# Kernel optimization log

Measured on AMD Instinct MI355X. Metric: run time of the kernel, lower is better.

Reference implementation:

```python
import jax, jax.numpy as jnp
import numpy as np

B, D, T = 32, 1024, 1000
LMAX = 200
VOCAB = 80
BLANK = VOCAB - 1
NEG = -1e30


def setup_inputs() -> dict:
    key = jax.random.key(0)
    ks = jax.random.split(key, 8)
    decoder_outputs = jax.random.normal(ks[0], (B, D, T), dtype=jnp.float32)
    target_text = jax.random.randint(ks[1], (B, LMAX), 0, BLANK, dtype=jnp.int32)
    decoder_lengths = jax.random.randint(ks[2], (B,), T // 2, T + 1, dtype=jnp.int32)
    target_lengths = jax.random.randint(ks[3], (B,), 1, LMAX + 1, dtype=jnp.int32)
    # learned params (dropout is identity in eval / deterministic reference)
    W1 = jax.random.normal(ks[4], (D, D), dtype=jnp.float32) * (1.0 / np.sqrt(D))
    b1 = jnp.zeros((D,), dtype=jnp.float32)
    W2 = jax.random.normal(ks[5], (D, VOCAB), dtype=jnp.float32) * (1.0 / np.sqrt(D))
    b2 = jnp.zeros((VOCAB,), dtype=jnp.float32)
    return {"decoder_outputs": decoder_outputs, "target_text": target_text,
            "decoder_lengths": decoder_lengths, "target_lengths": target_lengths,
            "W1": W1, "b1": b1, "W2": W2, "b2": b2}


def _ctc_nll(log_probs, targets, input_lengths, target_lengths):
    # log_probs: [T, B, V]; standard CTC alpha (forward) DP over extended labels.
    Tt, Bb, V = log_probs.shape
    L = targets.shape[1]
    S = 2 * L + 1
    ext = jnp.full((Bb, S), BLANK, dtype=targets.dtype).at[:, 1::2].set(targets)
    ext_m2 = jnp.pad(ext, ((0, 0), (2, 0)), constant_values=BLANK)[:, :S]
    allow_skip = (ext != BLANK) & (ext != ext_m2)
    allow_skip = allow_skip.at[:, :2].set(False)

    lp0 = log_probs[0]  # [B, V]
    alpha0 = jnp.full((Bb, S), NEG, dtype=log_probs.dtype)
    alpha0 = alpha0.at[:, 0].set(lp0[:, BLANK])
    alpha0 = alpha0.at[:, 1].set(jnp.take_along_axis(lp0, targets[:, :1], axis=1)[:, 0])

    def step(alpha, inp):
        lp_t, t = inp
        emit = jnp.take_along_axis(lp_t, ext, axis=1)  # [B, S]
        a2 = jnp.pad(alpha, ((0, 0), (1, 0)), constant_values=NEG)[:, :S]
        a3 = jnp.pad(alpha, ((0, 0), (2, 0)), constant_values=NEG)[:, :S]
        a3 = jnp.where(allow_skip, a3, NEG)
        new = jnp.logaddexp(jnp.logaddexp(alpha, a2), a3) + emit
        alpha = jnp.where((t < input_lengths)[:, None], new, alpha)
        return alpha, None

    alpha, _ = jax.lax.scan(step, alpha0, (log_probs[1:], jnp.arange(1, Tt)))
    i1 = (2 * target_lengths - 1)[:, None]
    i2 = (2 * target_lengths)[:, None]
    last = jnp.logaddexp(jnp.take_along_axis(alpha, i1, axis=1)[:, 0],
                         jnp.take_along_axis(alpha, i2, axis=1)[:, 0])
    nll = -last
    # zero_infinity=True: invalid alignments -> 0 loss
    return jnp.where(last > NEG / 2, nll, 0.0)


def reference(decoder_outputs, target_text, decoder_lengths, target_lengths, W1, b1, W2, b2):
    x = jnp.transpose(decoder_outputs, (0, 2, 1))          # [B, T, D]
    h = jax.nn.relu(jnp.einsum('btd,de->bte', x, W1) + b1)  # proj + ReLU (dropout=identity)
    logits = jnp.einsum('btd,dv->btv', h, W2) + b2          # [B, T, V]
    log_probs = jax.nn.log_softmax(logits, axis=2)
    log_probs = jnp.transpose(log_probs, (1, 0, 2))         # [T, B, V]
    ctc_loss = _ctc_nll(log_probs, target_text, decoder_lengths, target_lengths)
    return (ctc_loss / decoder_lengths.astype(jnp.float32)).mean()
```

## Files before the change

### kernel.cpp

```cpp
#include <hip/hip_runtime.h>
#include <cstdint>
#include <cstddef>

#define BN_ 32
#define DD_ 1024
#define TT_ 1000
#define LMAX_ 200
#define VC_ 80
#define BLANK_ 79
#define SS_ 401
#define SPAD 512
#define NEGV (-1e30f)

typedef _Float16 half8 __attribute__((ext_vector_type(8)));
typedef float f32x4 __attribute__((ext_vector_type(4)));

__device__ __forceinline__ void async16(const void* g, void* l) {
  __builtin_amdgcn_global_load_lds(
      (const __attribute__((address_space(1))) unsigned int*)g,
      (__attribute__((address_space(3))) unsigned int*)l, 16, 0, 0);
}

__global__ __launch_bounds__(256) void transpose_all_kernel(
    const float* __restrict__ dec, const float* __restrict__ W1,
    const float* __restrict__ W2, _Float16* __restrict__ Af,
    _Float16* __restrict__ W1T, _Float16* __restrict__ W2T) {
  __shared__ _Float16 T[64][72];
  int z = blockIdx.z;
  const float* in; _Float16* out; int C;
  const int R = 1024;
  if (z < 32) {
    in = dec + (size_t)z * R * TT_;
    out = Af + (size_t)z * TT_ * R;
    C = TT_;
  } else if (z == 32) {
    in = W1; out = W1T; C = 1024;
  } else {
    in = W2; out = W2T; C = VC_;
  }
  int c0 = blockIdx.x * 64, r0 = blockIdx.y * 64;
  if (c0 >= C) return;
  int tid = threadIdx.x;
  int cl = tid & 63, rg = tid >> 6;
  int c = c0 + cl;
  bool cv = (c < C);
  const float* ip = in + (size_t)(r0 + rg * 16) * C + c;
  _Float16 h[16];
#pragma unroll
  for (int i = 0; i < 16; ++i) h[i] = cv ? (_Float16)ip[(size_t)i * C] : (_Float16)0.f;
  *(half8*)&T[cl][rg * 16] = *(half8*)&h[0];
  *(half8*)&T[cl][rg * 16 + 8] = *(half8*)&h[8];
  __syncthreads();
  int cr = tid >> 2, rc = (tid & 3) * 16;
  if (c0 + cr < C) {
    half8 a = *(const half8*)&T[cr][rc];
    half8 b2 = *(const half8*)&T[cr][rc + 8];
    _Float16* op = out + (size_t)(c0 + cr) * R + r0 + rc;
    *(half8*)op = a;
    *(half8*)(op + 8) = b2;
  }
}

__device__ __forceinline__ void stage_half(const _Float16* __restrict__ X,
                                           int x0, int kt, int h,
                                           _Float16* lds, int tid, int K) {
#pragma unroll
  for (int jj = 0; jj < 2; ++jj) {
    int seg = tid + 512 * jj;
    int row = seg >> 3, slot = seg & 7;
    int cg = slot ^ (row & 7);
    async16(X + (size_t)(x0 + h * 128 + row) * K + kt * 64 + cg * 8,
            lds + seg * 8);
  }
}

__global__ __launch_bounds__(512, 2) void gemm_relu_kernel(
    const _Float16* __restrict__ A, const _Float16* __restrict__ Bt,
    const float* __restrict__ bias, _Float16* __restrict__ H,
    int M, int N, int K) {
  __shared__ __align__(16) _Float16 sA[2][16384];
  __shared__ __align__(16) _Float16 sB[2][16384];
  int tid = threadIdx.x;
  int wave = tid >> 6, lane = tid & 63;
  int quad = lane >> 4, r16 = lane & 15;
  int wm = wave >> 2, wn = wave & 3;

  int orig = blockIdx.x, nwg = gridDim.x;
  int xcd = orig & 7, loc = orig >> 3;
  int qq = nwg >> 3, rr = nwg & 7;
  int wg = (xcd < rr ? xcd * (qq + 1) : rr * (qq + 1) + (xcd - rr) * qq) + loc;
  int m0 = (wg >> 2) * 256, n0 = (wg & 3) * 256;

  f32x4 acc[4][8];
#pragma unroll
  for (int q = 0; q < 4; ++q)
#pragma unroll
    for (int f = 0; f < 8; ++f) acc[q][f] = {0.f, 0.f, 0.f, 0.f};

  stage_half(A, m0, 0, 0, &sA[0][0], tid, K);
  stage_half(A, m0, 0, 1, &sA[0][8192], tid, K);
  stage_half(Bt, n0, 0, 0, &sB[0][0], tid, K);
  stage_half(Bt, n0, 0, 1, &sB[0][8192], tid, K);
  stage_half(A, m0, 1, 0, &sA[1][0], tid, K);
  stage_half(Bt, n0, 1, 0, &sB[1][0], tid, K);
  stage_half(A, m0, 1, 1, &sA[1][8192], tid, K);
  asm volatile("s_waitcnt vmcnt(6)" ::: "memory");
  __builtin_amdgcn_s_barrier();

  const int NKT = K >> 6;
#pragma unroll 2
  for (int t = 0; t < NKT; ++t) {
    int cur = t & 1, nxt = cur ^ 1;
    int t1 = (t + 1 < NKT) ? t + 1 : NKT - 1;
    int t2 = (t + 2 < NKT) ? t + 2 : NKT - 1;
    const _Float16* As = sA[cur];
    const _Float16* Bs = sB[cur];
#pragma unroll
    for (int q = 0; q < 4; ++q) {
      const int qm = q >> 1, qn = q & 1;
      half8 af[4][2], bf[2][2];
      int abase = (qm * 128 + wm * 64 + r16) * 64;
      int bbase = (qn * 128 + wn * 32 + r16) * 64;
      int sw0 = ((0 * 4 + quad) ^ (r16 & 7)) * 8;
      int sw1 = ((1 * 4 + quad) ^ (r16 & 7)) * 8;
#pragma unroll
      for (int i = 0; i < 4; ++i) {
        af[i][0] = *(const half8*)&As[abase + i * 16 * 64 + sw0];
        af[i][1] = *(const half8*)&As[abase + i * 16 * 64 + sw1];
      }
#pragma unroll
      for (int j = 0; j < 2; ++j) {
        bf[j][0] = *(const half8*)&Bs[bbase + j * 16 * 64 + sw0];
        bf[j][1] = *(const half8*)&Bs[bbase + j * 16 * 64 + sw1];
      }
      if (q == 0) stage_half(Bt, n0, t1, 1, &sB[nxt][8192], tid, K);
      else if (q == 1) stage_half(A, m0, t2, 0, &sA[cur][0], tid, K);
      else if (q == 2) stage_half(Bt, n0, t2, 0, &sB[cur][0], tid, K);
      else stage_half(A, m0, t2, 1, &sA[cur][8192], tid, K);
      __builtin_amdgcn_s_barrier();
      asm volatile("s_waitcnt lgkmcnt(0)" ::: "memory");
      __builtin_amdgcn_s_setprio(1);
#pragma unroll
      for (int i = 0; i < 4; ++i)
#pragma unroll
        for (int j = 0; j < 2; ++j) {
          acc[q][i * 2 + j] = __builtin_amdgcn_mfma_f32_16x16x32_f16(
              af[i][0], bf[j][0], acc[q][i * 2 + j], 0, 0, 0);
          acc[q][i * 2 + j] = __builtin_amdgcn_mfma_f32_16x16x32_f16(
              af[i][1], bf[j][1], acc[q][i * 2 + j], 0, 0, 0);
        }
      __builtin_amdgcn_s_setprio(0);
      if (q == 3) asm volatile("s_waitcnt vmcnt(6)" ::: "memory");
      __builtin_amdgcn_s_barrier();
    }
  }
  asm volatile("s_waitcnt vmcnt(0)" ::: "memory");

  float bvv[2][2];
#pragma unroll
  for (int qn = 0; qn < 2; ++qn)
#pragma unroll
    for (int j = 0; j < 2; ++j)
      bvv[qn][j] = bias[n0 + qn * 128 + wn * 32 + j * 16 + r16];
#pragma unroll
  for (int q = 0; q < 4; ++q) {
    const int qm = q >> 1, qn = q & 1;
#pragma unroll
    for (int i = 0; i < 4; ++i)
#pragma unroll
      for (int j = 0; j < 2; ++j) {
#pragma unroll
        for (int r = 0; r < 4; ++r) {
          int m = m0 + qm * 128 + wm * 64 + i * 16 + quad * 4 + r;
          int n = n0 + qn * 128 + wn * 32 + j * 16 + r16;
          float v = acc[q][i * 2 + j][r] + bvv[qn][j];
          H[(size_t)m * N + n] = (_Float16)fmaxf(v, 0.f);
        }
      }
  }
}

__global__ __launch_bounds__(256) void gemm_prob_kernel(
    const _Float16* __restrict__ A, const _Float16* __restrict__ Bt,
    const float* __restrict__ bias, const int* __restrict__ targets,
    float* __restrict__ EM, int M, int K) {
  constexpr int BK = 64;
  __shared__ __align__(16) _Float16 sA[64 * BK];
  __shared__ __align__(16) _Float16 sB[VC_ * BK];
  __shared__ float sP[64][VC_];
  int tid = threadIdx.x;
  int wave = tid >> 6, lane = tid & 63;
  int quad = lane >> 4, r16 = lane & 15;
  int m0 = blockIdx.x * 64;

  f32x4 acc[5];
#pragma unroll
  for (int j = 0; j < 5; ++j) acc[j] = {0.f, 0.f, 0.f, 0.f};

  for (int kt = 0; kt < K; kt += BK) {
#pragma unroll
    for (int jj = 0; jj < 2; ++jj) {
      int seg = tid + 256 * jj;
      int row = seg >> 3, slot = seg & 7;
      int cg = slot ^ (row & 7);
      async16(A + (size_t)(m0 + row) * K + kt + cg * 8, &sA[seg * 8]);
    }
#pragma unroll
    for (int jj = 0; jj < 3; ++jj) {
      int seg = tid + 256 * jj;
      if (seg < VC_ * 8) {
        int row = seg >> 3, slot = seg & 7;
        int cg = slot ^ (row & 7);
        async16(Bt + (size_t)row * K + kt + cg * 8, &sB[seg * 8]);
      }
    }
    __syncthreads();
#pragma unroll
    for (int ku = 0; ku < 2; ++ku) {
      int sw = ((ku * 4 + quad) ^ (r16 & 7)) * 8;
      half8 af = *(const half8*)&sA[(wave * 16 + r16) * BK + sw];
      half8 bfr[5];
#pragma unroll
      for (int j = 0; j < 5; ++j)
        bfr[j] = *(const half8*)&sB[(j * 16 + r16) * BK + sw];
#pragma unroll
      for (int j = 0; j < 5; ++j)
        acc[j] = __builtin_amdgcn_mfma_f32_16x16x32_f16(af, bfr[j], acc[j], 0, 0, 0);
    }
    __syncthreads();
  }
  float bv[5];
#pragma unroll
  for (int j = 0; j < 5; ++j) bv[j] = bias[j * 16 + r16];
#pragma unroll
  for (int rr = 0; rr < 4; ++rr) {
    float vals[5];
    float mx = -3.4e38f;
#pragma unroll
    for (int j = 0; j < 5; ++j) {
      vals[j] = acc[j][rr] + bv[j];
      mx = fmaxf(mx, vals[j]);
    }
#pragma unroll
    for (int d = 1; d < 16; d <<= 1) mx = fmaxf(mx, __shfl_xor(mx, d));
    float ex[5], sm = 0.f;
#pragma unroll
    for (int j = 0; j < 5; ++j) { ex[j] = __expf(vals[j] - mx); sm += ex[j]; }
#pragma unroll
    for (int d = 1; d < 16; d <<= 1) sm += __shfl_xor(sm, d);
    float rinv = 1.f / sm;
    int ml = wave * 16 + quad * 4 + rr;
#pragma unroll
    for (int j = 0; j < 5; ++j) sP[ml][j * 16 + r16] = ex[j] * rinv;
  }
  __syncthreads();

  {
    int row = tid >> 2, s0 = (tid & 3) * 128;
    int m = m0 + row;
    int b = m / TT_;
    const int* tg = targets + b * LMAX_;
    const float* pr = sP[row];
    float pb = pr[BLANK_];
    float* o = EM + (size_t)m * SPAD + s0;
#pragma unroll 4
    for (int sc = 0; sc < 128; sc += 4) {
      int s = s0 + sc;
      float4 vv;
      vv.x = (s + 0 < SS_) ? pb : 0.f;
      vv.y = (s + 1 < SS_) ? pr[tg[(s + 1) >> 1]] : 0.f;
      vv.z = (s + 2 < SS_) ? pb : 0.f;
      vv.w = (s + 3 < SS_) ? pr[tg[(s + 3) >> 1]] : 0.f;
      *(float4*)o = vv;
      o += 4;
    }
  }
}

__device__ __forceinline__ void dp_step_fwd(float (&bta)[8], int& k,
                                            const f32x4 e0, const f32x4 e1,
                                            const float (&am)[4], int lane) {
  float pm1 = __shfl_up(bta[7], 1);
  int pk = __shfl_up(k, 1);
  if (lane == 0) { pm1 = 0.f; pk = k; }
  int knew = max(k, pk);
  pm1 = ldexpf(pm1, pk - knew);
  int ds = k - knew;
#pragma unroll
  for (int r = 0; r < 8; ++r) bta[r] = ldexpf(bta[r], ds);
  k = knew;
  float nb[8];
  nb[0] = (bta[0] + pm1) * e0.x;
  nb[1] = fmaf(am[0], pm1, bta[1] + bta[0]) * e0.y;
  nb[2] = (bta[2] + bta[1]) * e0.z;
  nb[3] = fmaf(am[1], bta[1], bta[3] + bta[2]) * e0.w;
  nb[4] = (bta[4] + bta[3]) * e1.x;
  nb[5] = fmaf(am[2], bta[3], bta[5] + bta[4]) * e1.y;
  nb[6] = (bta[6] + bta[5]) * e1.z;
  nb[7] = fmaf(am[3], bta[5], bta[7] + bta[6]) * e1.w;
#pragma unroll
  for (int r = 0; r < 8; ++r) bta[r] = nb[r];
}

__device__ __forceinline__ void dp_step_bwd(float (&g)[8], int& k,
                                            const f32x4 e0, const f32x4 e1,
                                            const float (&amB)[4], int lane) {
  float gh[8];
  gh[0] = g[0] * e0.x; gh[1] = g[1] * e0.y;
  gh[2] = g[2] * e0.z; gh[3] = g[3] * e0.w;
  gh[4] = g[4] * e1.x; gh[5] = g[5] * e1.y;
  gh[6] = g[6] * e1.z; gh[7] = g[7] * e1.w;
  float qm1 = __shfl_down(gh[0], 1);
  float qm2 = __shfl_down(gh[1], 1);
  int nk = __shfl_down(k, 1);
  if (lane == 63) { qm1 = 0.f; qm2 = 0.f; nk = k; }
  int knew = max(k, nk);
  int dq = nk - knew;
  qm1 = ldexpf(qm1, dq);
  qm2 = ldexpf(qm2, dq);
  int ds = k - knew;
#pragma unroll
  for (int r = 0; r < 8; ++r) gh[r] = ldexpf(gh[r], ds);
  k = knew;
  g[0] = gh[0] + gh[1];
  g[1] = fmaf(amB[0], gh[3], gh[1] + gh[2]);
  g[2] = gh[2] + gh[3];
  g[3] = fmaf(amB[1], gh[5], gh[3] + gh[4]);
  g[4] = gh[4] + gh[5];
  g[5] = fmaf(amB[2], gh[7], gh[5] + gh[6]);
  g[6] = gh[6] + gh[7];
  g[7] = fmaf(amB[3], qm2, gh[7] + qm1);
}

__device__ __forceinline__ void dp_rescale(float (&v)[8], int& k) {
  float m = fmaxf(fmaxf(fmaxf(v[0], v[1]), fmaxf(v[2], v[3])),
                  fmaxf(fmaxf(v[4], v[5]), fmaxf(v[6], v[7])));
  int ex = (__float_as_int(m) >> 23) - 126;
  k += ex;
#pragma unroll
  for (int r = 0; r < 8; ++r) v[r] = ldexpf(v[r], -ex);
}

__device__ __forceinline__ float allow_f(const int* __restrict__ tg, int s) {
  if (!(s & 1) || s < 3) return 0.f;
  int li = s >> 1;
  if (li >= LMAX_) return 0.f;
  int lab = tg[li];
  return (lab != BLANK_ && lab != tg[li - 1]) ? 1.f : 0.f;
}

__global__ __launch_bounds__(128) void ctc_dp_kernel(
    const float* __restrict__ EM, const int* __restrict__ targets,
    const int* __restrict__ dlen, const int* __restrict__ tlen,
    float* __restrict__ out) {
  __shared__ float sg[SPAD];
  __shared__ int skg[64];
  int b = blockIdx.x;
  int wave = threadIdx.x >> 6;
  int lane = threadIdx.x & 63;
  const float* em = EM + (size_t)b * TT_ * SPAD + lane * 8;
  const int* tg = targets + b * LMAX_;
  int Tl = dlen[b], Ll = tlen[b];
  int tm = Tl >> 1;

  constexpr int PD = 8;
  f32x4 pf[PD][2];
  float v[8];
  int k = 0;

  if (wave == 0) {
    float am[4];
#pragma unroll
    for (int j = 0; j < 4; ++j) am[j] = allow_f(tg, lane * 8 + 2 * j + 1);
    f32x4 r0a = *(const f32x4*)(em);
#pragma unroll
    for (int r = 0; r < 8; ++r) v[r] = 0.f;
    if (lane == 0) { v[0] = r0a.x; v[1] = r0a.y; }
#pragma unroll
    for (int j = 0; j < PD; ++j) {
      int ri = min(1 + j, TT_ - 1);
      pf[j][0] = *(const f32x4*)(em + (size_t)ri * SPAD);
      pf[j][1] = *(const f32x4*)(em + (size_t)ri * SPAD + 4);
    }
    int t = 1;
    for (; t + (PD - 1) <= tm; t += PD) {
#pragma unroll
      for (int u = 0; u < PD; ++u) {
        dp_step_fwd(v, k, pf[u][0], pf[u][1], am, lane);
        if (u & 1) dp_rescale(v, k);
        int ri = min(t + u + PD, TT_ - 1);
        pf[u][0] = *(const f32x4*)(em + (size_t)ri * SPAD);
        pf[u][1] = *(const f32x4*)(em + (size_t)ri * SPAD + 4);
      }
    }
#pragma unroll
    for (int u = 0; u < PD; ++u) {
      if (t + u <= tm) {
        dp_step_fwd(v, k, pf[u][0], pf[u][1], am, lane);
        if (u & 1) dp_rescale(v, k);
      }
    }
  } else {
    float amB[4];
#pragma unroll
    for (int j = 0; j < 4; ++j) amB[j] = allow_f(tg, lane * 8 + 2 * j + 3);
    int s1 = 2 * Ll - 1, s2 = 2 * Ll;
#pragma unroll
    for (int r = 0; r < 8; ++r) {
      int s = lane * 8 + r;
      v[r] = (s == s1 || s == s2) ? 1.f : 0.f;
    }
#pragma unroll
    for (int j = 0; j < PD; ++j) {
      int ri = max(Tl - 1 - j, 0);
      pf[j][0] = *(const f32x4*)(em + (size_t)ri * SPAD);
      pf[j][1] = *(const f32x4*)(em + (size_t)ri * SPAD + 4);
    }
    int t = Tl - 1;
    for (; t - (PD - 1) > tm; t -= PD) {
#pragma unroll
      for (int u = 0; u < PD; ++u) {
        dp_step_bwd(v, k, pf[u][0], pf[u][1], amB, lane);
        if (u & 1) dp_rescale(v, k);
        int ri = max(t - u - PD, 0);
        pf[u][0] = *(const f32x4*)(em + (size_t)ri * SPAD);
        pf[u][1] = *(const f32x4*)(em + (size_t)ri * SPAD + 4);
      }
    }
#pragma unroll
    for (int u = 0; u < PD; ++u) {
      if (t - u > tm) {
        dp_step_bwd(v, k, pf[u][0], pf[u][1], amB, lane);
        if (u & 1) dp_rescale(v, k);
      }
    }
#pragma unroll
    for (int r = 0; r < 8; ++r) sg[lane * 8 + r] = v[r];
    skg[lane] = k;
  }
  __syncthreads();
  if (wave == 0) {
    float p = 0.f;
#pragma unroll
    for (int r = 0; r < 8; ++r) p = fmaf(v[r], sg[lane * 8 + r], p);
    int kk = k + skg[lane];
    if (p == 0.f) kk = -(1 << 30);
#pragma unroll
    for (int d = 1; d < 64; d <<= 1) {
      float po = __shfl_xor(p, d);
      int ko = __shfl_xor(kk, d);
      int km = max(kk, ko);
      p = ldexpf(p, kk - km) + ldexpf(po, ko - km);
      kk = km;
    }
    if (lane == 0) {
      float nll = 0.f;
      if (p > 0.f) nll = -((log2f(p) + (float)kk) * 0.69314718055994531f);
      atomicAdd(out, nll / (float)Tl * (1.f / BN_));
    }
  }
}

extern "C" void kernel_launch(void* const* d_in, const int* in_sizes, int n_in,
                              void* d_out, int out_size, void* d_ws, size_t ws_size,
                              hipStream_t stream) {
  const float* dec = (const float*)d_in[0];
  const int* tgt   = (const int*)d_in[1];
  const int* dln   = (const int*)d_in[2];
  const int* tln   = (const int*)d_in[3];
  const float* W1  = (const float*)d_in[4];
  const float* b1  = (const float*)d_in[5];
  const float* W2  = (const float*)d_in[6];
  const float* b2  = (const float*)d_in[7];
  float* out = (float*)d_out;

  char* ws = (char*)d_ws;
  const size_t M = (size_t)BN_ * TT_;
  _Float16* Af   = (_Float16*)(ws);
  float* EM      = (float*)(ws);
  _Float16* Hf   = (_Float16*)(ws + 65536000);
  _Float16* W1T  = (_Float16*)(ws + 131072000);
  _Float16* W2T  = (_Float16*)(ws + 133169152);

  hipMemsetAsync(d_out, 0, sizeof(float), stream);

  transpose_all_kernel<<<dim3(16, 16, 34), 256, 0, stream>>>(
      dec, W1, W2, Af, W1T, W2T);
  gemm_relu_kernel<<<dim3((1024 / 256) * (M / 256), 1, 1), 512, 0, stream>>>(
      Af, W1T, b1, Hf, (int)M, DD_, DD_);
  gemm_prob_kernel<<<dim3(M / 64, 1, 1), 256, 0, stream>>>(
      Hf, W2T, b2, tgt, EM, (int)M, DD_);
  ctc_dp_kernel<<<dim3(BN_, 1, 1), 128, 0, stream>>>(EM, tgt, dln, tln, out);
}
```

Measured before the change: 413.9 us.

## Give each wave a contiguous 128x64 subtile and restage by K-half phases

Changes the wave-to-output mapping of the first GEMM so each wave owns a contiguous 128x64 tile instead of four scattered 64x32 quadrants. B fragments are loaded once per K-substep and reused across both M halves, which reduces LDS reads per MFMA. The loop is restructured into two-tile iterations with a new prefetch order that stages A and B halves in four phases, and the vmcnt thresholds are adjusted to match. This increases fragment reuse but changes the pipelining order and wait counts, so correctness depends on those counts being right.

```diff
diff --git a/kernel.cpp b/kernel.cpp
--- a/kernel.cpp
+++ b/kernel.cpp
@@ -91,93 +91,95 @@
   int wg = (xcd < rr ? xcd * (qq + 1) : rr * (qq + 1) + (xcd - rr) * qq) + loc;
   int m0 = (wg >> 2) * 256, n0 = (wg & 3) * 256;
 
-  f32x4 acc[4][8];
-#pragma unroll
-  for (int q = 0; q < 4; ++q)
-#pragma unroll
-    for (int f = 0; f < 8; ++f) acc[q][f] = {0.f, 0.f, 0.f, 0.f};
-
-  stage_half(A, m0, 0, 0, &sA[0][0], tid, K);
-  stage_half(A, m0, 0, 1, &sA[0][8192], tid, K);
+  f32x4 acc[2][4][4];
+#pragma unroll
+  for (int mh = 0; mh < 2; ++mh)
+#pragma unroll
+    for (int i = 0; i < 4; ++i)
+#pragma unroll
+      for (int j = 0; j < 4; ++j) acc[mh][i][j] = {0.f, 0.f, 0.f, 0.f};
+
   stage_half(Bt, n0, 0, 0, &sB[0][0], tid, K);
   stage_half(Bt, n0, 0, 1, &sB[0][8192], tid, K);
-  stage_half(A, m0, 1, 0, &sA[1][0], tid, K);
+  stage_half(A,  m0, 0, 0, &sA[0][0], tid, K);
+  stage_half(A,  m0, 0, 1, &sA[0][8192], tid, K);
   stage_half(Bt, n0, 1, 0, &sB[1][0], tid, K);
-  stage_half(A, m0, 1, 1, &sA[1][8192], tid, K);
-  asm volatile("s_waitcnt vmcnt(6)" ::: "memory");
+  stage_half(Bt, n0, 1, 1, &sB[1][8192], tid, K);
+  asm volatile("s_waitcnt vmcnt(4)" ::: "memory");
   __builtin_amdgcn_s_barrier();
 
   const int NKT = K >> 6;
-#pragma unroll 2
-  for (int t = 0; t < NKT; ++t) {
-    int cur = t & 1, nxt = cur ^ 1;
-    int t1 = (t + 1 < NKT) ? t + 1 : NKT - 1;
-    int t2 = (t + 2 < NKT) ? t + 2 : NKT - 1;
-    const _Float16* As = sA[cur];
-    const _Float16* Bs = sB[cur];
-#pragma unroll
-    for (int q = 0; q < 4; ++q) {
-      const int qm = q >> 1, qn = q & 1;
-      half8 af[4][2], bf[2][2];
-      int abase = (qm * 128 + wm * 64 + r16) * 64;
-      int bbase = (qn * 128 + wn * 32 + r16) * 64;
-      int sw0 = ((0 * 4 + quad) ^ (r16 & 7)) * 8;
-      int sw1 = ((1 * 4 + quad) ^ (r16 & 7)) * 8;
-#pragma unroll
-      for (int i = 0; i < 4; ++i) {
-        af[i][0] = *(const half8*)&As[abase + i * 16 * 64 + sw0];
-        af[i][1] = *(const half8*)&As[abase + i * 16 * 64 + sw1];
-      }
-#pragma unroll
-      for (int j = 0; j < 2; ++j) {
-        bf[j][0] = *(const half8*)&Bs[bbase + j * 16 * 64 + sw0];
-        bf[j][1] = *(const half8*)&Bs[bbase + j * 16 * 64 + sw1];
-      }
-      if (q == 0) stage_half(Bt, n0, t1, 1, &sB[nxt][8192], tid, K);
-      else if (q == 1) stage_half(A, m0, t2, 0, &sA[cur][0], tid, K);
-      else if (q == 2) stage_half(Bt, n0, t2, 0, &sB[cur][0], tid, K);
-      else stage_half(A, m0, t2, 1, &sA[cur][8192], tid, K);
-      __builtin_amdgcn_s_barrier();
-      asm volatile("s_waitcnt lgkmcnt(0)" ::: "memory");
-      __builtin_amdgcn_s_setprio(1);
-#pragma unroll
-      for (int i = 0; i < 4; ++i)
-#pragma unroll
-        for (int j = 0; j < 2; ++j) {
-          acc[q][i * 2 + j] = __builtin_amdgcn_mfma_f32_16x16x32_f16(
-              af[i][0], bf[j][0], acc[q][i * 2 + j], 0, 0, 0);
-          acc[q][i * 2 + j] = __builtin_amdgcn_mfma_f32_16x16x32_f16(
-              af[i][1], bf[j][1], acc[q][i * 2 + j], 0, 0, 0);
+#pragma unroll 1
+  for (int it = 0; it < (NKT >> 1); ++it) {
+    int T1 = 2 * it + 1;
+    int F0 = min(2 * it + 2, NKT - 1);
+    int F1 = min(2 * it + 3, NKT - 1);
+#pragma unroll
+    for (int tt = 0; tt < 2; ++tt) {
+      const _Float16* As = sA[tt];
+      const _Float16* Bs = sB[tt];
+      half8 bf[4];
+#pragma unroll
+      for (int ku = 0; ku < 2; ++ku) {
+#pragma unroll
+        for (int mh = 0; mh < 2; ++mh) {
+          int sw = ((ku * 4 + quad) ^ (r16 & 7)) * 8;
+          half8 af[4];
+#pragma unroll
+          for (int i = 0; i < 4; ++i)
+            af[i] = *(const half8*)&As[(wm * 128 + mh * 64 + i * 16 + r16) * 64 + sw];
+          if (mh == 0) {
+#pragma unroll
+            for (int j = 0; j < 4; ++j)
+              bf[j] = *(const half8*)&Bs[(wn * 64 + j * 16 + r16) * 64 + sw];
+          }
+          const int ph = ku * 2 + mh;
+          if (tt == 0) {
+            if (ph == 0)      stage_half(A,  m0, T1, 0, &sA[1][0], tid, K);
+            else if (ph == 1) stage_half(A,  m0, T1, 1, &sA[1][8192], tid, K);
+            else if (ph == 2) stage_half(Bt, n0, F0, 0, &sB[0][0], tid, K);
+            else              stage_half(Bt, n0, F0, 1, &sB[0][8192], tid, K);
+          } else {
+            if (ph == 0)      stage_half(A,  m0, F0, 0, &sA[0][0], tid, K);
+            else if (ph == 1) stage_half(A,  m0, F0, 1, &sA[0][8192], tid, K);
+            else if (ph == 2) stage_half(Bt, n0, F1, 0, &sB[1][0], tid, K);
+            else              stage_half(Bt, n0, F1, 1, &sB[1][8192], tid, K);
+          }
+          __builtin_amdgcn_s_barrier();
+          asm volatile("s_waitcnt lgkmcnt(0)" ::: "memory");
+          __builtin_amdgcn_s_setprio(1);
+#pragma unroll
+          for (int i = 0; i < 4; ++i)
+#pragma unroll
+            for (int j = 0; j < 4; ++j)
+              acc[mh][i][j] = __builtin_amdgcn_mfma_f32_16x16x32_f16(
+                  af[i], bf[j], acc[mh][i][j], 0, 0, 0);
+          __builtin_amdgcn_s_setprio(0);
+          if (ph == 3) asm volatile("s_waitcnt vmcnt(4)" ::: "memory");
+          __builtin_amdgcn_s_barrier();
         }
-      __builtin_amdgcn_s_setprio(0);
-      if (q == 3) asm volatile("s_waitcnt vmcnt(6)" ::: "memory");
-      __builtin_amdgcn_s_barrier();
+      }
     }
   }
   asm volatile("s_waitcnt vmcnt(0)" ::: "memory");
 
-  float bvv[2][2];
-#pragma unroll
-  for (int qn = 0; qn < 2; ++qn)
-#pragma unroll
-    for (int j = 0; j < 2; ++j)
-      bvv[qn][j] = bias[n0 + qn * 128 + wn * 32 + j * 16 + r16];
-#pragma unroll
-  for (int q = 0; q < 4; ++q) {
-    const int qm = q >> 1, qn = q & 1;
+  float bvv[4];
+#pragma unroll
+  for (int j = 0; j < 4; ++j) bvv[j] = bias[n0 + wn * 64 + j * 16 + r16];
+#pragma unroll
+  for (int mh = 0; mh < 2; ++mh)
 #pragma unroll
     for (int i = 0; i < 4; ++i)
 #pragma unroll
-      for (int j = 0; j < 2; ++j) {
+      for (int j = 0; j < 4; ++j) {
 #pragma unroll
         for (int r = 0; r < 4; ++r) {
-          int m = m0 + qm * 128 + wm * 64 + i * 16 + quad * 4 + r;
-          int n = n0 + qn * 128 + wn * 32 + j * 16 + r16;
-          float v = acc[q][i * 2 + j][r] + bvv[qn][j];
+          int m = m0 + wm * 128 + mh * 64 + i * 16 + quad * 4 + r;
+          int n = n0 + wn * 64 + j * 16 + r16;
+          float v = acc[mh][i][j][r] + bvv[j];
           H[(size_t)m * N + n] = (_Float16)fmaxf(v, 0.f);
         }
       }
-  }
 }
 
 __global__ __launch_bounds__(256) void gemm_prob_kernel(
```

Result: no change. 415.8 us (+0.4%).
